# Optimization experiments

Measured on AMD Instinct MI355X. Metric: run time of the kernel, lower is better.

## Reference

```python
import jax, jax.numpy as jnp
import numpy as np

B, S, D = 4, 2048, 1024
H, HD = 16, 64  # num_head, head_dim


def setup_inputs() -> dict:
    key = jax.random.key(0)
    k0, k1, k2, k3, k4 = jax.random.split(key, 5)
    scale = 1.0 / np.sqrt(D)
    return {
        "x": jax.random.normal(k0, (B, S, D), dtype=jnp.float32),
        "Wq": jax.random.normal(k1, (D, H * HD), dtype=jnp.float32) * scale,
        "Wk": jax.random.normal(k2, (D, H * HD), dtype=jnp.float32) * scale,
        "Wv": jax.random.normal(k3, (D, H * HD), dtype=jnp.float32) * scale,
        "Wo": jax.random.normal(k4, (H * HD, H * HD), dtype=jnp.float32) * scale,
    }


def reference(x, Wq, Wk, Wv, Wo):
    b, s, _ = x.shape
    # projections -> [b, h, s, hd]
    q = (x @ Wq).reshape(b, s, H, HD).transpose(0, 2, 1, 3)
    k = (x @ Wk).reshape(b, s, H, HD).transpose(0, 2, 1, 3)
    v = (x @ Wv).reshape(b, s, H, HD).transpose(0, 2, 1, 3)
    # scaled scores [b, h, s, s]
    scores = jnp.einsum("bhqd,bhkd->bhqk", q, k) / np.sqrt(HD).astype(np.float32)
    causal = jnp.triu(jnp.ones((s, s), dtype=bool), k=1)  # True above diagonal
    scores = jnp.where(causal, -jnp.inf, scores)
    att = jax.nn.softmax(scores, axis=-1)
    # dropout p=0.0 -> identity
    out = jnp.einsum("bhqk,bhkd->bqhd", att, v).reshape(b, s, H * HD)
    return out @ Wo
```

## Files before the change

kernel.cpp:

```cpp
#include <hip/hip_runtime.h>


typedef __attribute__((ext_vector_type(8))) short short8_t;
typedef __attribute__((ext_vector_type(4))) short short4_t;
typedef __attribute__((ext_vector_type(4))) float float4_t;

constexpr int Bz = 4, Sq = 2048, Dm = 1024, NH = 16, HD = 64;
constexpr int LDSPITCH = 72;

#define GLOAD_LDS16(g, l)                                                      \
  __builtin_amdgcn_global_load_lds(                                            \
      (const __attribute__((address_space(1))) unsigned int*)(g),              \
      (__attribute__((address_space(3))) unsigned int*)(l), 16, 0, 0)

__device__ __forceinline__ unsigned short f2bf(float f) {
  unsigned u = __builtin_bit_cast(unsigned, f);
  u += 0x7fffu + ((u >> 16) & 1u);
  return (unsigned short)(u >> 16);
}

__device__ __forceinline__ float exp2_fast(float x) {
#if __has_builtin(__builtin_amdgcn_exp2f)
  return __builtin_amdgcn_exp2f(x);
#else
  return exp2f(x);
#endif
}

__global__ __launch_bounds__(256) void cast_x_kernel(const float* __restrict__ x,
                                                     unsigned short* __restrict__ xb) {
  size_t i = (size_t)blockIdx.x * 256 + threadIdx.x;
  float4 v = ((const float4*)x)[i];
  ushort4 o;
  o.x = f2bf(v.x); o.y = f2bf(v.y); o.z = f2bf(v.z); o.w = f2bf(v.w);
  ((ushort4*)xb)[i] = o;
}

__global__ __launch_bounds__(256) void transpose_w_kernel(
    const float* __restrict__ Wq, const float* __restrict__ Wk,
    const float* __restrict__ Wv, const float* __restrict__ Wo,
    unsigned short* __restrict__ wqT, unsigned short* __restrict__ wkT,
    unsigned short* __restrict__ wvT, unsigned short* __restrict__ woT) {
  __shared__ float tile[64][65];
  int zz = blockIdx.z;
  const float* W = zz == 0 ? Wq : (zz == 1 ? Wk : (zz == 2 ? Wv : Wo));
  unsigned short* WT = zz == 0 ? wqT : (zz == 1 ? wkT : (zz == 2 ? wvT : woT));
  int n0 = blockIdx.x * 64, k0 = blockIdx.y * 64;
  int tx = threadIdx.x & 63, ty = threadIdx.x >> 6;
#pragma unroll
  for (int i = 0; i < 16; ++i) {
    int r = i * 4 + ty;
    tile[r][tx] = W[(size_t)(k0 + r) * Dm + n0 + tx];
  }
  __syncthreads();
#pragma unroll
  for (int i = 0; i < 16; ++i) {
    int r = i * 4 + ty;
    WT[(size_t)(n0 + r) * Dm + k0 + tx] = f2bf(tile[tx][r]);
  }
}

__device__ __forceinline__ void gemm_mainloop(const unsigned short* __restrict__ A,
                                              const unsigned short* __restrict__ BT,
                                              int m0, int n0,
                                              unsigned short* lA, unsigned short* lB,
                                              float4_t acc[4][4]) {
  const int tid = threadIdx.x;
  const int lane = tid & 63, lr = lane & 15, quad = lane >> 4;
  const int wave = tid >> 6;
  const int mw = (wave >> 1) * 64, nw = (wave & 1) * 64;
  const int srow = tid >> 3;
  const int scol = (tid & 7) * 8;
  const unsigned short* ga = A + (size_t)(m0 + srow) * Dm + scol;
  const unsigned short* gb = BT + (size_t)(n0 + srow) * Dm + scol;
  unsigned short* la = lA + tid * 8;
  unsigned short* lb = lB + tid * 8;

  for (int k0 = 0; k0 < Dm; k0 += 64) {
    __syncthreads();
#pragma unroll
    for (int iss = 0; iss < 4; ++iss) {
      GLOAD_LDS16(ga + (size_t)iss * 32 * Dm + k0, la + iss * 32 * 64);
      GLOAD_LDS16(gb + (size_t)iss * 32 * Dm + k0, lb + iss * 32 * 64);
    }
    __syncthreads();
#pragma unroll
    for (int kk = 0; kk < 2; ++kk) {
      short8_t a[4], b[4];
#pragma unroll
      for (int i = 0; i < 4; ++i)
        a[i] = *(const short8_t*)(lA + (mw + i * 16 + lr) * 64 + kk * 32 + quad * 8);
#pragma unroll
      for (int j = 0; j < 4; ++j)
        b[j] = *(const short8_t*)(lB + (nw + j * 16 + lr) * 64 + kk * 32 + quad * 8);
#pragma unroll
      for (int i = 0; i < 4; ++i)
#pragma unroll
        for (int j = 0; j < 4; ++j)
          acc[i][j] = __builtin_amdgcn_mfma_f32_16x16x32_bf16(a[i], b[j], acc[i][j], 0, 0, 0);
    }
  }
}

__global__ __launch_bounds__(256) void gemm_qkv_kernel(
    const unsigned short* __restrict__ xb,
    const unsigned short* __restrict__ wqT, const unsigned short* __restrict__ wkT,
    const unsigned short* __restrict__ wvT,
    unsigned short* __restrict__ qb, unsigned short* __restrict__ kb,
    unsigned short* __restrict__ vt) {
  __shared__ unsigned short lA[128 * 64];
  __shared__ unsigned short lB[128 * 64];
  const unsigned short* WT = blockIdx.z == 0 ? wqT : (blockIdx.z == 1 ? wkT : wvT);
  unsigned short* outb = blockIdx.z == 0 ? qb : (blockIdx.z == 1 ? kb : vt);
  bool isV = blockIdx.z == 2;
  int lane = threadIdx.x & 63, wave = threadIdx.x >> 6;
  int lr = lane & 15, quad = lane >> 4;
  int m0 = blockIdx.y * 128, n0 = blockIdx.x * 128;
  int m_base = m0 + (wave >> 1) * 64;
  int n_base = n0 + (wave & 1) * 64;
  float4_t z = {0.f, 0.f, 0.f, 0.f};
  float4_t acc[4][4];
#pragma unroll
  for (int i = 0; i < 4; ++i)
#pragma unroll
    for (int j = 0; j < 4; ++j) acc[i][j] = z;
  gemm_mainloop(xb, WT, m0, n0, lA, lB, acc);
  if (isV) {
#pragma unroll
    for (int i = 0; i < 4; ++i)
#pragma unroll
      for (int j = 0; j < 4; ++j) {
        int m = m_base + i * 16 + quad * 4;
        int n = n_base + j * 16 + lr;
        int b = m >> 11, s = m & (Sq - 1);
        int h = n >> 6, hd = n & (HD - 1);
        ushort4 pk;
        pk.x = f2bf(acc[i][j][0]); pk.y = f2bf(acc[i][j][1]);
        pk.z = f2bf(acc[i][j][2]); pk.w = f2bf(acc[i][j][3]);
        *(ushort4*)(outb + (((size_t)b * NH + h) * HD + hd) * Sq + s) = pk;
      }
  } else {
#pragma unroll
    for (int i = 0; i < 4; ++i)
#pragma unroll
      for (int j = 0; j < 4; ++j)
#pragma unroll
        for (int r = 0; r < 4; ++r) {
          int m = m_base + i * 16 + quad * 4 + r;
          int n = n_base + j * 16 + lr;
          int b = m >> 11, s = m & (Sq - 1);
          int h = n >> 6, hd = n & (HD - 1);
          outb[(((size_t)b * NH + h) * Sq + s) * HD + hd] = f2bf(acc[i][j][r]);
        }
  }
}

__global__ __launch_bounds__(256) void gemm_out_kernel(
    const unsigned short* __restrict__ ao, const unsigned short* __restrict__ woT,
    float* __restrict__ out) {
  __shared__ unsigned short lA[128 * 64];
  __shared__ unsigned short lB[128 * 64];
  int lane = threadIdx.x & 63, wave = threadIdx.x >> 6;
  int lr = lane & 15, quad = lane >> 4;
  int m0 = blockIdx.y * 128, n0 = blockIdx.x * 128;
  int m_base = m0 + (wave >> 1) * 64;
  int n_base = n0 + (wave & 1) * 64;
  float4_t z = {0.f, 0.f, 0.f, 0.f};
  float4_t acc[4][4];
#pragma unroll
  for (int i = 0; i < 4; ++i)
#pragma unroll
    for (int j = 0; j < 4; ++j) acc[i][j] = z;
  gemm_mainloop(ao, woT, m0, n0, lA, lB, acc);
#pragma unroll
  for (int i = 0; i < 4; ++i)
#pragma unroll
    for (int j = 0; j < 4; ++j)
#pragma unroll
      for (int r = 0; r < 4; ++r) {
        int m = m_base + i * 16 + quad * 4 + r;
        int n = n_base + j * 16 + lr;
        out[(size_t)m * Dm + n] = acc[i][j][r];
      }
}

__global__ __launch_bounds__(256) void attn_kernel(
    const unsigned short* __restrict__ qbuf, const unsigned short* __restrict__ kbuf,
    const unsigned short* __restrict__ vtbuf, unsigned short* __restrict__ ao) {
  __shared__ unsigned short lk[64 * LDSPITCH];
  __shared__ unsigned short lv[64 * LDSPITCH];
  int bh = blockIdx.x;
  int ti = 31 - (int)blockIdx.y;
  int wave = threadIdx.x >> 6, lane = threadIdx.x & 63;
  int lcol = lane & 15, quad = lane >> 4;
  const unsigned short* Q = qbuf + (size_t)bh * Sq * HD;
  const unsigned short* K = kbuf + (size_t)bh * Sq * HD;
  const unsigned short* Vt = vtbuf + (size_t)bh * HD * Sq;
  int b = bh >> 4, h = bh & 15;
  int srow = threadIdx.x >> 2;
  int scol = (threadIdx.x & 3) * 16;
  float4_t z = {0.f, 0.f, 0.f, 0.f};
  constexpr float kS = 0.18033688011112042f;

  int q0w = ti * 64 + wave * 16;
  int q_global = q0w + lcol;
  short8_t qf0 = *(const short8_t*)(Q + (size_t)(q0w + lcol) * HD + quad * 8);
  short8_t qf1 = *(const short8_t*)(Q + (size_t)(q0w + lcol) * HD + 32 + quad * 8);
  float m_i = -INFINITY, l_i = 0.f;
  float4_t o[4];
#pragma unroll
  for (int f = 0; f < 4; ++f) o[f] = z;

  int nkt = ti + 1;
  for (int kt = 0; kt < nkt; ++kt) {
    int key0 = kt * 64;
    __syncthreads();
    {
      const unsigned short* kg = K + (size_t)(key0 + srow) * HD + scol;
      const unsigned short* vg = Vt + (size_t)srow * Sq + key0 + scol;
      unsigned short* kl = lk + srow * LDSPITCH + scol;
      unsigned short* vl = lv + srow * LDSPITCH + scol;
      *(short8_t*)(kl) = *(const short8_t*)(kg);
      *(short8_t*)(kl + 8) = *(const short8_t*)(kg + 8);
      *(short8_t*)(vl) = *(const short8_t*)(vg);
      *(short8_t*)(vl + 8) = *(const short8_t*)(vg + 8);
    }
    __syncthreads();

    bool need_mask = (key0 + 63 > q0w);
    float s[16];
    float tmax = -INFINITY;
#pragma unroll
    for (int s4 = 0; s4 < 4; ++s4) {
      short8_t kf0 = *(const short8_t*)(lk + (s4 * 16 + lcol) * LDSPITCH + quad * 8);
      short8_t kf1 = *(const short8_t*)(lk + (s4 * 16 + lcol) * LDSPITCH + 32 + quad * 8);
      float4_t st = z;
      st = __builtin_amdgcn_mfma_f32_16x16x32_bf16(kf0, qf0, st, 0, 0, 0);
      st = __builtin_amdgcn_mfma_f32_16x16x32_bf16(kf1, qf1, st, 0, 0, 0);
#pragma unroll
      for (int r = 0; r < 4; ++r) {
        float v = st[r] * kS;
        if (need_mask && (key0 + s4 * 16 + quad * 4 + r > q_global)) v = -INFINITY;
        s[s4 * 4 + r] = v;
        tmax = fmaxf(tmax, v);
      }
    }
    tmax = fmaxf(tmax, __shfl_xor(tmax, 16, 64));
    tmax = fmaxf(tmax, __shfl_xor(tmax, 32, 64));

    if (__any(tmax > m_i + 8.f)) {
      float m_new = fmaxf(m_i, tmax);
      float alpha = exp2_fast(m_i - m_new);
      l_i *= alpha;
      m_i = m_new;
      float at[4];
#pragma unroll
      for (int r = 0; r < 4; ++r) at[r] = __shfl(alpha, quad * 4 + r, 64);
#pragma unroll
      for (int f = 0; f < 4; ++f)
#pragma unroll
        for (int r = 0; r < 4; ++r) o[f][r] *= at[r];
    }

    float psum = 0.f;
    short4_t pf[4];
#pragma unroll
    for (int s4 = 0; s4 < 4; ++s4) {
      float p0 = exp2_fast(s[s4 * 4 + 0] - m_i);
      float p1 = exp2_fast(s[s4 * 4 + 1] - m_i);
      float p2 = exp2_fast(s[s4 * 4 + 2] - m_i);
      float p3 = exp2_fast(s[s4 * 4 + 3] - m_i);
      psum += (p0 + p1) + (p2 + p3);
      unsigned lo, hi;
      asm("v_cvt_pk_bf16_f32 %0, %1, %2" : "=v"(lo) : "v"(p0), "v"(p1));
      asm("v_cvt_pk_bf16_f32 %0, %1, %2" : "=v"(hi) : "v"(p2), "v"(p3));
      uint2 packed;
      packed.x = lo;
      packed.y = hi;
      pf[s4] = __builtin_bit_cast(short4_t, packed);
    }
    psum += __shfl_xor(psum, 16, 64);
    psum += __shfl_xor(psum, 32, 64);
    l_i += psum;

#pragma unroll
    for (int f = 0; f < 4; ++f)
#pragma unroll
      for (int s4 = 0; s4 < 4; ++s4) {
        short4_t vf =
            *(const short4_t*)(lv + (f * 16 + lcol) * LDSPITCH + s4 * 16 + quad * 4);
        o[f] = __builtin_amdgcn_mfma_f32_16x16x16bf16_1k(pf[s4], vf, o[f], 0, 0, 0);
      }
  }

  float lt[4];
#pragma unroll
  for (int r = 0; r < 4; ++r) lt[r] = 1.f / __shfl(l_i, quad * 4 + r, 64);
#pragma unroll
  for (int f = 0; f < 4; ++f)
#pragma unroll
    for (int r = 0; r < 4; ++r) {
      int q = q0w + quad * 4 + r;
      int hd = f * 16 + lcol;
      ao[((size_t)b * Sq + q) * (NH * HD) + h * HD + hd] = f2bf(o[f][r] * lt[r]);
    }
}

extern "C" void kernel_launch(void* const* d_in, const int* in_sizes, int n_in,
                              void* d_out, int out_size, void* d_ws, size_t ws_size,
                              hipStream_t stream) {
  const float* x = (const float*)d_in[0];
  const float* Wq = (const float*)d_in[1];
  const float* Wk = (const float*)d_in[2];
  const float* Wv = (const float*)d_in[3];
  const float* Wo = (const float*)d_in[4];
  float* out = (float*)d_out;

  char* ws = (char*)d_ws;
  size_t off = 0;
  auto carve = [&](size_t bytes) {
    void* p = ws + off;
    off += (bytes + 255) & ~(size_t)255;
    return p;
  };
  const size_t xe = (size_t)Bz * Sq * Dm;
  const size_t we = (size_t)Dm * Dm;
  unsigned short* xb = (unsigned short*)carve(xe * 2);
  unsigned short* wqT = (unsigned short*)carve(we * 2);
  unsigned short* wkT = (unsigned short*)carve(we * 2);
  unsigned short* wvT = (unsigned short*)carve(we * 2);
  unsigned short* woT = (unsigned short*)carve(we * 2);
  unsigned short* qb = (unsigned short*)carve(xe * 2);
  unsigned short* kb = (unsigned short*)carve(xe * 2);
  unsigned short* vt = (unsigned short*)carve(xe * 2);
  unsigned short* ao = (unsigned short*)carve(xe * 2);
  (void)ws_size;

  cast_x_kernel<<<xe / 4 / 256, 256, 0, stream>>>(x, xb);
  transpose_w_kernel<<<dim3(16, 16, 4), 256, 0, stream>>>(Wq, Wk, Wv, Wo,
                                                          wqT, wkT, wvT, woT);
  gemm_qkv_kernel<<<dim3(8, 64, 3), 256, 0, stream>>>(xb, wqT, wkT, wvT, qb, kb, vt);
  attn_kernel<<<dim3(Bz * NH, 32), 256, 0, stream>>>(qb, kb, vt, ao);
  gemm_out_kernel<<<dim3(8, 64), 256, 0, stream>>>(ao, woT, out);
}
```

Before: 285.2 us.

## Use direct global-to-LDS loads with XOR swizzle in attention; fold softmax scale into Q

Attention K/V tiles are now loaded with global_load_lds straight into an unpadded LDS layout that is XOR-swizzled, replacing register-staged copies into a padded layout. Fragment reads use matching swizzled offsets so bank conflicts stay low. The softmax scale (1/sqrt(d)·log2e) moves into the Q projection epilogue, which removes a multiply per score, and the row max uses three-input max trees. Folding the scale before the bf16 rounding of Q changes rounding slightly.

```diff
diff --git a/kernel.cpp b/kernel.cpp
--- a/kernel.cpp
+++ b/kernel.cpp
@@ -6,7 +6,6 @@
 typedef __attribute__((ext_vector_type(4))) float float4_t;
 
 constexpr int Bz = 4, Sq = 2048, Dm = 1024, NH = 16, HD = 64;
-constexpr int LDSPITCH = 72;
 
 #define GLOAD_LDS16(g, l)                                                      \
   __builtin_amdgcn_global_load_lds(                                            \
@@ -25,6 +24,10 @@
 #else
   return exp2f(x);
 #endif
+}
+
+__device__ __forceinline__ float m3(float a, float b, float c) {
+  return fmaxf(fmaxf(a, b), c);
 }
 
 __global__ __launch_bounds__(256) void cast_x_kernel(const float* __restrict__ x,
@@ -113,6 +116,7 @@
   const unsigned short* WT = blockIdx.z == 0 ? wqT : (blockIdx.z == 1 ? wkT : wvT);
   unsigned short* outb = blockIdx.z == 0 ? qb : (blockIdx.z == 1 ? kb : vt);
   bool isV = blockIdx.z == 2;
+  float qscale = (blockIdx.z == 0) ? 0.18033688011112042f : 1.0f;
   int lane = threadIdx.x & 63, wave = threadIdx.x >> 6;
   int lr = lane & 15, quad = lane >> 4;
   int m0 = blockIdx.y * 128, n0 = blockIdx.x * 128;
@@ -150,7 +154,7 @@
           int n = n_base + j * 16 + lr;
           int b = m >> 11, s = m & (Sq - 1);
           int h = n >> 6, hd = n & (HD - 1);
-          outb[(((size_t)b * NH + h) * Sq + s) * HD + hd] = f2bf(acc[i][j][r]);
+          outb[(((size_t)b * NH + h) * Sq + s) * HD + hd] = f2bf(acc[i][j][r] * qscale);
         }
   }
 }
@@ -187,20 +191,35 @@
 __global__ __launch_bounds__(256) void attn_kernel(
     const unsigned short* __restrict__ qbuf, const unsigned short* __restrict__ kbuf,
     const unsigned short* __restrict__ vtbuf, unsigned short* __restrict__ ao) {
-  __shared__ unsigned short lk[64 * LDSPITCH];
-  __shared__ unsigned short lv[64 * LDSPITCH];
+  __shared__ unsigned short lk[64 * 64];
+  __shared__ unsigned short lv[64 * 64];
+  int tid = threadIdx.x;
   int bh = blockIdx.x;
   int ti = 31 - (int)blockIdx.y;
-  int wave = threadIdx.x >> 6, lane = threadIdx.x & 63;
+  int wave = tid >> 6, lane = tid & 63;
   int lcol = lane & 15, quad = lane >> 4;
+  int lc7 = lcol & 7;
   const unsigned short* Q = qbuf + (size_t)bh * Sq * HD;
   const unsigned short* K = kbuf + (size_t)bh * Sq * HD;
   const unsigned short* Vt = vtbuf + (size_t)bh * HD * Sq;
   int b = bh >> 4, h = bh & 15;
-  int srow = threadIdx.x >> 2;
-  int scol = (threadIdx.x & 3) * 16;
   float4_t z = {0.f, 0.f, 0.f, 0.f};
-  constexpr float kS = 0.18033688011112042f;
+
+  const int r0 = tid >> 3;
+  const int sg = (tid & 7) ^ (r0 & 7);
+  const unsigned short* kg_base = K + (size_t)r0 * HD + sg * 8;
+  const unsigned short* vg_base = Vt + (size_t)r0 * Sq + sg * 8;
+  unsigned short* kl0 = lk + tid * 8;
+  unsigned short* kl1 = lk + 2048 + tid * 8;
+  unsigned short* vl0 = lv + tid * 8;
+  unsigned short* vl1 = lv + 2048 + tid * 8;
+
+  const int koff0 = (quad ^ lc7) * 8;
+  const int koff1 = ((quad | 4) ^ lc7) * 8;
+  int voff[4];
+#pragma unroll
+  for (int s4 = 0; s4 < 4; ++s4)
+    voff[s4] = (((s4 * 2 + (quad >> 1)) ^ lc7) * 8) + (quad & 1) * 4;
 
   int q0w = ti * 64 + wave * 16;
   int q_global = q0w + lcol;
@@ -216,35 +235,40 @@
     int key0 = kt * 64;
     __syncthreads();
     {
-      const unsigned short* kg = K + (size_t)(key0 + srow) * HD + scol;
-      const unsigned short* vg = Vt + (size_t)srow * Sq + key0 + scol;
-      unsigned short* kl = lk + srow * LDSPITCH + scol;
-      unsigned short* vl = lv + srow * LDSPITCH + scol;
-      *(short8_t*)(kl) = *(const short8_t*)(kg);
-      *(short8_t*)(kl + 8) = *(const short8_t*)(kg + 8);
-      *(short8_t*)(vl) = *(const short8_t*)(vg);
-      *(short8_t*)(vl + 8) = *(const short8_t*)(vg + 8);
+      const unsigned short* kg = kg_base + (size_t)key0 * HD;
+      const unsigned short* vg = vg_base + key0;
+      GLOAD_LDS16(kg, kl0);
+      GLOAD_LDS16(kg + (size_t)32 * HD, kl1);
+      GLOAD_LDS16(vg, vl0);
+      GLOAD_LDS16(vg + (size_t)32 * Sq, vl1);
     }
     __syncthreads();
 
     bool need_mask = (key0 + 63 > q0w);
     float s[16];
-    float tmax = -INFINITY;
 #pragma unroll
     for (int s4 = 0; s4 < 4; ++s4) {
-      short8_t kf0 = *(const short8_t*)(lk + (s4 * 16 + lcol) * LDSPITCH + quad * 8);
-      short8_t kf1 = *(const short8_t*)(lk + (s4 * 16 + lcol) * LDSPITCH + 32 + quad * 8);
+      const unsigned short* kr = lk + (s4 * 16 + lcol) * 64;
+      short8_t kf0 = *(const short8_t*)(kr + koff0);
+      short8_t kf1 = *(const short8_t*)(kr + koff1);
       float4_t st = z;
       st = __builtin_amdgcn_mfma_f32_16x16x32_bf16(kf0, qf0, st, 0, 0, 0);
       st = __builtin_amdgcn_mfma_f32_16x16x32_bf16(kf1, qf1, st, 0, 0, 0);
 #pragma unroll
       for (int r = 0; r < 4; ++r) {
-        float v = st[r] * kS;
+        float v = st[r];
         if (need_mask && (key0 + s4 * 16 + quad * 4 + r > q_global)) v = -INFINITY;
         s[s4 * 4 + r] = v;
-        tmax = fmaxf(tmax, v);
       }
     }
+    float ta = m3(s[0], s[1], s[2]);
+    float tb = m3(s[3], s[4], s[5]);
+    float tc = m3(s[6], s[7], s[8]);
+    float td = m3(s[9], s[10], s[11]);
+    float te = m3(s[12], s[13], s[14]);
+    float tmax = m3(ta, tb, tc);
+    tmax = m3(tmax, td, te);
+    tmax = fmaxf(tmax, s[15]);
     tmax = fmaxf(tmax, __shfl_xor(tmax, 16, 64));
     tmax = fmaxf(tmax, __shfl_xor(tmax, 32, 64));
 
@@ -284,13 +308,14 @@
     l_i += psum;
 
 #pragma unroll
-    for (int f = 0; f < 4; ++f)
+    for (int f = 0; f < 4; ++f) {
+      const unsigned short* vr = lv + (f * 16 + lcol) * 64;
 #pragma unroll
       for (int s4 = 0; s4 < 4; ++s4) {
-        short4_t vf =
-            *(const short4_t*)(lv + (f * 16 + lcol) * LDSPITCH + s4 * 16 + quad * 4);
+        short4_t vf = *(const short4_t*)(vr + voff[s4]);
         o[f] = __builtin_amdgcn_mfma_f32_16x16x16bf16_1k(pf[s4], vf, o[f], 0, 0, 0);
       }
+    }
   }
 
   float lt[4];
```

Result: no change. 280.6 us (-1.6%).
